# Optimization experiments

Hardware: AMD Instinct MI355X
Metric: run time of the kernel (lower is better)

Reference implementation:

```python
import jax, jax.numpy as jnp
import numpy as np
import math

D = 768
SCALE = math.sqrt(D)


def setup_inputs() -> dict:
    key = jax.random.key(0)
    k1, k2, k3, k4 = jax.random.split(key, 4)
    lhs = jax.random.normal(k1, (8, 1024, D), dtype=jnp.float32)
    rhs = jax.random.normal(k2, (8, 1024, D), dtype=jnp.float32)
    # xavier_normal_ std = sqrt(2/(fan_in+fan_out))
    std = math.sqrt(2.0 / (D + D))
    W_lhs = jax.random.normal(k3, (D, D), dtype=jnp.float32) * std
    W_rhs = jax.random.normal(k4, (D, D), dtype=jnp.float32) * std
    return {"lhs": lhs, "rhs": rhs, "W_lhs": W_lhs, "W_rhs": W_rhs}


def reference(lhs, rhs, W_lhs, W_rhs):
    # Linear (no bias): x @ W.T, then tanh
    l = jnp.tanh(jnp.einsum('nld,ed->nle', lhs, W_lhs))  # (N, L, D)
    r = jnp.tanh(jnp.einsum('nrd,ed->nre', rhs, W_rhs))  # (N, R, D)
    scores = jnp.einsum('nld,nrd->nlr', l, r)            # (N, L, R)
    attn_lhs = jax.nn.softmax(scores, axis=2)            # unscaled, row softmax
    attn_rhs = jax.nn.softmax(scores / SCALE, axis=1)    # scaled, column softmax
    out_lhs = jnp.einsum('nlr,nrd->nld', attn_lhs, rhs)
    out_rhs = jnp.einsum('nlr,nld->nrd', attn_rhs, lhs)
    return (jnp.concatenate([lhs, out_lhs], axis=2),
            jnp.concatenate([rhs, out_rhs], axis=2))
```

## Files before the change

kernel.cpp:

```cpp
#include <hip/hip_runtime.h>

typedef _Float16 f16_t;
typedef _Float16 f16x4 __attribute__((ext_vector_type(4)));
typedef _Float16 f16x8 __attribute__((ext_vector_type(8)));
typedef short s16x8 __attribute__((ext_vector_type(8)));
typedef unsigned short u16x4 __attribute__((ext_vector_type(4)));
typedef float floatx4 __attribute__((ext_vector_type(4)));

#define NB 8
#define SEQ 1024
#define DIM 768
#define INV_SCALE 0.03608439182435161f
#define ROW_SHIFT 40.0f

__device__ inline unsigned short f2bf(float f) {
  unsigned u = __builtin_bit_cast(unsigned, f);
  u += 0x7fffu + ((u >> 16) & 1u);
  return (unsigned short)(u >> 16);
}

__device__ inline void async_load16(const void* g, void* l) {
  __builtin_amdgcn_global_load_lds((__attribute__((address_space(1))) void*)g,
                                   (__attribute__((address_space(3))) void*)l,
                                   16, 0, 0);
}


__global__ __launch_bounds__(256, 3) void gemm_proj(
    const f16_t* __restrict__ A0, const f16_t* __restrict__ W0,
    const f16_t* __restrict__ A1, const f16_t* __restrict__ W1,
    f16_t* __restrict__ C0, f16_t* __restrict__ C1) {
  __shared__ __align__(16) f16_t sA[128 * 64];
  __shared__ __align__(16) f16_t sB[128 * 64];
  const int b = blockIdx.x;
  const int xcd = b & 7, slot = b >> 3;
  const int grp = slot / 6, j = slot - grp * 6;
  const int stripe = grp * 8 + xcd;
  const int z = stripe >> 6, my = stripe & 63;
  const f16_t* Ab = (z ? A1 : A0) + (size_t)my * 128 * DIM;
  const f16_t* Bb = (z ? W1 : W0) + (size_t)j * 128 * DIM;
  f16_t* C = z ? C1 : C0;
  const int tid = threadIdx.x;
  const int lane = tid & 63;
  const int wave = tid >> 6;
  const int wr = wave >> 1, wc = wave & 1;
  const int fr = lane & 15;
  const int fq = lane >> 4;
  const int swz = ((lane & 7) ^ (lane >> 3)) << 3;
  const int x7 = (fr & 7) << 3;

  floatx4 acc[4][4] = {};

  for (int kt = 0; kt < DIM; kt += 64) {
    #pragma unroll
    for (int i = 0; i < 4; ++i) {
      const int ch = i * 4 + wave;
      const int row = ch * 8 + (lane >> 3);
      const size_t g = (size_t)row * DIM + kt + swz;
      async_load16(Ab + g, (char*)sA + ch * 1024);
      async_load16(Bb + g, (char*)sB + ch * 1024);
    }
    __syncthreads();
    #pragma unroll
    for (int ks = 0; ks < 64; ks += 32) {
      f16x8 af[4], bf[4];
      #pragma unroll
      for (int t = 0; t < 4; ++t) {
        const int cs = (ks + fq * 8) ^ x7;
        af[t] = *(const f16x8*)&sA[(wr * 64 + t * 16 + fr) * 64 + cs];
        bf[t] = *(const f16x8*)&sB[(wc * 64 + t * 16 + fr) * 64 + cs];
      }
      #pragma unroll
      for (int ti = 0; ti < 4; ++ti)
        #pragma unroll
        for (int tj = 0; tj < 4; ++tj)
          acc[ti][tj] = __builtin_amdgcn_mfma_f32_16x16x32_f16(
              af[ti], bf[tj], acc[ti][tj], 0, 0, 0);
    }
    __syncthreads();
  }

  const size_t m0 = (size_t)my * 128, n0 = (size_t)j * 128;
  #pragma unroll
  for (int ti = 0; ti < 4; ++ti)
    #pragma unroll
    for (int tj = 0; tj < 4; ++tj) {
      const size_t gm = m0 + wr * 64 + ti * 16 + fq * 4;
      const size_t gn = n0 + wc * 64 + tj * 16 + fr;
      #pragma unroll
      for (int i = 0; i < 4; ++i)
        C[(gm + i) * DIM + gn] = (f16_t)tanhf(acc[ti][tj][i]);
    }
}

__global__ __launch_bounds__(256, 3) void gemm_scores(
    const f16_t* __restrict__ A, const f16_t* __restrict__ B,
    unsigned short* __restrict__ e_l, f16_t* __restrict__ e_rT,
    float* __restrict__ rowpart, float* __restrict__ colpart) {
  __shared__ __align__(16) f16_t sA[128 * 64];
  __shared__ __align__(16) f16_t sB[128 * 64];
  const int b = blockIdx.x;
  const int xcd = b & 7, slot = b >> 3;
  const int grp = slot >> 3, j = slot & 7;
  const int stripe = grp * 8 + xcd;
  const int z = stripe >> 3, my = stripe & 7;
  const f16_t* Ab = A + (size_t)z * SEQ * DIM + (size_t)my * 128 * DIM;
  const f16_t* Bb = B + (size_t)z * SEQ * DIM + (size_t)j * 128 * DIM;
  const int tid = threadIdx.x;
  const int lane = tid & 63;
  const int wave = tid >> 6;
  const int wr = wave >> 1, wc = wave & 1;
  const int fr = lane & 15;
  const int fq = lane >> 4;
  const int swz = ((lane & 7) ^ (lane >> 3)) << 3;
  const int x7 = (fr & 7) << 3;

  floatx4 acc[4][4] = {};

  for (int kt = 0; kt < DIM; kt += 64) {
    #pragma unroll
    for (int i = 0; i < 4; ++i) {
      const int ch = i * 4 + wave;
      const int row = ch * 8 + (lane >> 3);
      const size_t g = (size_t)row * DIM + kt + swz;
      async_load16(Ab + g, (char*)sA + ch * 1024);
      async_load16(Bb + g, (char*)sB + ch * 1024);
    }
    __syncthreads();
    #pragma unroll
    for (int ks = 0; ks < 64; ks += 32) {
      f16x8 af[4], bf[4];
      #pragma unroll
      for (int t = 0; t < 4; ++t) {
        const int cs = (ks + fq * 8) ^ x7;
        af[t] = *(const f16x8*)&sA[(wr * 64 + t * 16 + fr) * 64 + cs];
        bf[t] = *(const f16x8*)&sB[(wc * 64 + t * 16 + fr) * 64 + cs];
      }
      #pragma unroll
      for (int ti = 0; ti < 4; ++ti)
        #pragma unroll
        for (int tj = 0; tj < 4; ++tj)
          acc[ti][tj] = __builtin_amdgcn_mfma_f32_16x16x32_f16(
              af[ti], bf[tj], acc[ti][tj], 0, 0, 0);
    }
    __syncthreads();
  }

  const size_t m0 = (size_t)my * 128, n0 = (size_t)j * 128;
  unsigned short* eL = e_l + (size_t)z * SEQ * SEQ;
  f16_t* eT = e_rT + (size_t)z * SEQ * SEQ;
  float* srow = (float*)sA;
  float* scol = (float*)sB;

  #pragma unroll
  for (int ti = 0; ti < 4; ++ti) {
    #pragma unroll
    for (int i = 0; i < 4; ++i) {
      const size_t row = m0 + wr * 64 + ti * 16 + fq * 4 + i;
      float s = 0.f;
      #pragma unroll
      for (int tj = 0; tj < 4; ++tj) {
        const float e = __expf(acc[ti][tj][i] - ROW_SHIFT);
        s += e;
        eL[row * SEQ + n0 + wc * 64 + tj * 16 + fr] = f2bf(e);
      }
      s += __shfl_xor(s, 1, 64);
      s += __shfl_xor(s, 2, 64);
      s += __shfl_xor(s, 4, 64);
      s += __shfl_xor(s, 8, 64);
      if (fr == 0) srow[wc * 128 + wr * 64 + ti * 16 + fq * 4 + i] = s;
    }
  }
  #pragma unroll
  for (int tj = 0; tj < 4; ++tj) {
    const size_t coln = n0 + wc * 64 + tj * 16 + fr;
    float s = 0.f;
    #pragma unroll
    for (int ti = 0; ti < 4; ++ti) {
      f16x4 ev;
      #pragma unroll
      for (int i = 0; i < 4; ++i) {
        const float e = __expf(acc[ti][tj][i] * INV_SCALE);
        s += e;
        ev[i] = (f16_t)e;
      }
      *(f16x4*)&eT[coln * SEQ + m0 + wr * 64 + ti * 16 + fq * 4] = ev;
    }
    s += __shfl_xor(s, 16, 64);
    s += __shfl_xor(s, 32, 64);
    if (fq == 0) scol[wr * 128 + wc * 64 + tj * 16 + fr] = s;
  }
  __syncthreads();
  if (tid < 128)
    rowpart[((size_t)(z * 8 + j)) * SEQ + my * 128 + tid] =
        srow[tid] + srow[128 + tid];
  else
    colpart[((size_t)(z * 8 + my)) * SEQ + j * 128 + (tid - 128)] =
        scol[tid - 128] + scol[tid];
}

template <bool BF>
__device__ __forceinline__ void apply_body(
    const f16_t* __restrict__ Ab, const f16_t* __restrict__ Bb,
    float* __restrict__ C, const float* __restrict__ pp, f16_t* sA, f16_t* sB,
    float* sinv) {
  const int tid = threadIdx.x;
  const int lane = tid & 63;
  const int wave = tid >> 6;
  const int wr = wave >> 1, wc = wave & 1;
  const int fr = lane & 15;
  const int fq = lane >> 4;
  const int swz = ((lane & 7) ^ (lane >> 3)) << 3;
  const int x7 = (fr & 7) << 3;

  if (tid < 128) {
    float s = 0.f;
    #pragma unroll
    for (int k = 0; k < 8; ++k) s += pp[k * SEQ + tid];
    sinv[tid] = 1.f / s;
  }

  floatx4 acc[4][4] = {};

  for (int kt = 0; kt < SEQ; kt += 64) {
    #pragma unroll
    for (int i = 0; i < 4; ++i) {
      const int ch = i * 4 + wave;
      const int row = ch * 8 + (lane >> 3);
      const size_t g = (size_t)row * SEQ + kt + swz;
      async_load16(Ab + g, (char*)sA + ch * 1024);
      async_load16(Bb + g, (char*)sB + ch * 1024);
    }
    __syncthreads();
    #pragma unroll
    for (int ks = 0; ks < 64; ks += 32) {
      const int cs = (ks + fq * 8) ^ x7;
      #pragma unroll
      for (int ti = 0; ti < 4; ++ti) {
        const f16_t* pa = &sA[(wr * 64 + ti * 16 + fr) * 64 + cs];
        #pragma unroll
        for (int tj = 0; tj < 4; ++tj) {
          const f16_t* pb = &sB[(wc * 64 + tj * 16 + fr) * 64 + cs];
          if constexpr (BF)
            acc[ti][tj] = __builtin_amdgcn_mfma_f32_16x16x32_bf16(
                *(const s16x8*)pa, *(const s16x8*)pb, acc[ti][tj], 0, 0, 0);
          else
            acc[ti][tj] = __builtin_amdgcn_mfma_f32_16x16x32_f16(
                *(const f16x8*)pa, *(const f16x8*)pb, acc[ti][tj], 0, 0, 0);
        }
      }
    }
    __syncthreads();
  }

  #pragma unroll
  for (int ti = 0; ti < 4; ++ti) {
    const int gm = wr * 64 + ti * 16 + fq * 4;
    const floatx4 iv = *(const floatx4*)&sinv[gm];
    #pragma unroll
    for (int tj = 0; tj < 4; ++tj) {
      const int gn = wc * 64 + tj * 16 + fr;
      #pragma unroll
      for (int i = 0; i < 4; ++i)
        C[(size_t)(gm + i) * (2 * DIM) + gn] = acc[ti][tj][i] * iv[i];
    }
  }
}

__global__ __launch_bounds__(256, 3) void gemm_apply(
    const f16_t* __restrict__ e_l, const f16_t* __restrict__ e_rT,
    const f16_t* __restrict__ rhsT, const f16_t* __restrict__ lhsT,
    const float* __restrict__ rowpart, const float* __restrict__ colpart,
    float* __restrict__ out0, float* __restrict__ out1) {
  __shared__ __align__(16) f16_t sA[128 * 64];
  __shared__ __align__(16) f16_t sB[128 * 64];
  __shared__ __align__(16) float sinv[128];
  const int b = blockIdx.x;
  const int xcd = b & 7, slot = b >> 3;
  const int grp = slot / 6, j = slot - grp * 6;
  const int stripe = grp * 8 + xcd;
  const int z = stripe >> 3, my = stripe & 7;
  const int n = z & 7;
  const size_t m0 = (size_t)my * 128, n0 = (size_t)j * 128;
  if (z < 8) {
    apply_body<true>(e_l + (size_t)n * SEQ * SEQ + m0 * SEQ,
                     rhsT + (size_t)n * SEQ * DIM + n0 * SEQ,
                     out0 + (size_t)n * SEQ * 2 * DIM + DIM + m0 * 2 * DIM + n0,
                     rowpart + (size_t)n * 8 * SEQ + m0, sA, sB, sinv);
  } else {
    apply_body<false>(
        e_rT + (size_t)n * SEQ * SEQ + m0 * SEQ,
        lhsT + (size_t)n * SEQ * DIM + n0 * SEQ,
        out1 + (size_t)n * SEQ * 2 * DIM + DIM + m0 * 2 * DIM + n0,
        colpart + (size_t)n * 8 * SEQ + m0, sA, sB, sinv);
  }
}

__global__ __launch_bounds__(256) void prep(
    const float* __restrict__ lhs, const float* __restrict__ rhs,
    const float* __restrict__ Wl, const float* __restrict__ Wr,
    f16_t* __restrict__ lf, f16_t* __restrict__ rf, f16_t* __restrict__ lhsT,
    unsigned short* __restrict__ rhsT, f16_t* __restrict__ Wlh,
    f16_t* __restrict__ Wrh, float* __restrict__ o0, float* __restrict__ o1) {
  const int z = blockIdx.z;
  const int tid = threadIdx.x;
  const int x4 = (tid & 15) * 4, ty = tid >> 4;
  const int c0 = blockIdx.x * 64, r0 = blockIdx.y * 64;
  if (z >= 16) {
    if (blockIdx.y >= 12) return;
    const float* in = (z == 17 ? Wr : Wl);
    f16_t* out = (z == 17 ? Wrh : Wlh);
    #pragma unroll
    for (int it = 0; it < 4; ++it) {
      const int row = r0 + ty + it * 16;
      const float4 v = *(const float4*)&in[(size_t)row * DIM + c0 + x4];
      f16x4 h = {(f16_t)v.x, (f16_t)v.y, (f16_t)v.z, (f16_t)v.w};
      *(f16x4*)&out[(size_t)row * DIM + c0 + x4] = h;
    }
    return;
  }
  __shared__ float tile[64][65];
  const int n = z & 7;
  const float* in = (z < 8 ? lhs : rhs) + (size_t)n * SEQ * DIM;
  f16_t* fout = (z < 8 ? lf : rf) + (size_t)n * SEQ * DIM;
  float* oh = (z < 8 ? o0 : o1) + (size_t)n * SEQ * 2 * DIM;
  #pragma unroll
  for (int it = 0; it < 4; ++it) {
    const int row = ty + it * 16;
    const float4 v = *(const float4*)&in[(size_t)(r0 + row) * DIM + c0 + x4];
    f16x4 h = {(f16_t)v.x, (f16_t)v.y, (f16_t)v.z, (f16_t)v.w};
    *(f16x4*)&fout[(size_t)(r0 + row) * DIM + c0 + x4] = h;
    *(float4*)&oh[(size_t)(r0 + row) * 2 * DIM + c0 + x4] = v;
    tile[row][x4 + 0] = v.x;
    tile[row][x4 + 1] = v.y;
    tile[row][x4 + 2] = v.z;
    tile[row][x4 + 3] = v.w;
  }
  __syncthreads();
  if (z < 8) {
    f16_t* T = lhsT + (size_t)n * SEQ * DIM;
    #pragma unroll
    for (int it = 0; it < 4; ++it) {
      const int cr = ty + it * 16;
      f16x4 o = {(f16_t)tile[x4 + 0][cr], (f16_t)tile[x4 + 1][cr],
                 (f16_t)tile[x4 + 2][cr], (f16_t)tile[x4 + 3][cr]};
      *(f16x4*)&T[(size_t)(c0 + cr) * SEQ + r0 + x4] = o;
    }
  } else {
    unsigned short* T = rhsT + (size_t)n * SEQ * DIM;
    #pragma unroll
    for (int it = 0; it < 4; ++it) {
      const int cr = ty + it * 16;
      u16x4 o = {f2bf(tile[x4 + 0][cr]), f2bf(tile[x4 + 1][cr]),
                 f2bf(tile[x4 + 2][cr]), f2bf(tile[x4 + 3][cr])};
      *(u16x4*)&T[(size_t)(c0 + cr) * SEQ + r0 + x4] = o;
    }
  }
}

extern "C" void kernel_launch(void* const* d_in, const int* in_sizes, int n_in,
                              void* d_out, int out_size, void* d_ws,
                              size_t ws_size, hipStream_t stream) {
  const float* lhs = (const float*)d_in[0];
  const float* rhs = (const float*)d_in[1];
  const float* Wl = (const float*)d_in[2];
  const float* Wr = (const float*)d_in[3];
  float* out0 = (float*)d_out;
  float* out1 = out0 + (size_t)NB * SEQ * (2 * DIM);

  char* ws = (char*)d_ws;
  f16_t* lhsT = (f16_t*)(ws + 0);
  unsigned short* rhsT = (unsigned short*)(ws + 12582912);
  f16_t* l_f = (f16_t*)(ws + 25165824);
  f16_t* r_f = (f16_t*)(ws + 37748736);
  f16_t* lhs_f = (f16_t*)(ws + 50331648);
  f16_t* rhs_f = (f16_t*)(ws + 62914560);
  f16_t* Wl_h = (f16_t*)(ws + 75497472);
  f16_t* Wr_h = (f16_t*)(ws + 76677120);
  unsigned short* e_l = (unsigned short*)(ws + 50331648);
  f16_t* e_rT = (f16_t*)(ws + 67108864);
  float* rowpart = (float*)(ws + 83886080);
  float* colpart = (float*)(ws + 84148224);

  prep<<<dim3(12, 16, 18), 256, 0, stream>>>(lhs, rhs, Wl, Wr, lhs_f, rhs_f,
                                             lhsT, rhsT, Wl_h, Wr_h, out0,
                                             out1);
  gemm_proj<<<768, 256, 0, stream>>>(lhs_f, Wl_h, rhs_f, Wr_h, l_f, r_f);
  gemm_scores<<<512, 256, 0, stream>>>(l_f, r_f, e_l, e_rT, rowpart, colpart);
  gemm_apply<<<768, 256, 0, stream>>>((const f16_t*)e_l, e_rT,
                                      (const f16_t*)rhsT, lhsT, rowpart,
                                      colpart, out0, out1);
}
```

Before: 251.3 us.

## Move transposes into scores kernel, stage e_rT via LDS, simplify prep

Takes the lhs/rhs transposes out of the prep kernel and runs them as extra blocks inside the scores kernel, so that memory-bound work overlaps the compute-bound score GEMM. The e_rT transposed store now goes through a swizzled shared-memory tile, giving 16-byte coalesced writes. Row and column partial sums are written per wave-half (16 partials), which drops the shared-memory reduction. Block-to-XCD mapping is changed so that each batch sits on one XCD, and tanh is computed with exp plus rcp. The risks are uncoalesced scalar transpose stores in the new blocks and some precision loss from the approximate tanh.

```diff
diff --git a/kernel.cpp b/kernel.cpp
--- a/kernel.cpp
+++ b/kernel.cpp
@@ -4,7 +4,6 @@
 typedef _Float16 f16x4 __attribute__((ext_vector_type(4)));
 typedef _Float16 f16x8 __attribute__((ext_vector_type(8)));
 typedef short s16x8 __attribute__((ext_vector_type(8)));
-typedef unsigned short u16x4 __attribute__((ext_vector_type(4)));
 typedef float floatx4 __attribute__((ext_vector_type(4)));
 
 #define NB 8
@@ -33,13 +32,15 @@
   __shared__ __align__(16) f16_t sA[128 * 64];
   __shared__ __align__(16) f16_t sB[128 * 64];
   const int b = blockIdx.x;
-  const int xcd = b & 7, slot = b >> 3;
-  const int grp = slot / 6, j = slot - grp * 6;
-  const int stripe = grp * 8 + xcd;
-  const int z = stripe >> 6, my = stripe & 63;
-  const f16_t* Ab = (z ? A1 : A0) + (size_t)my * 128 * DIM;
-  const f16_t* Bb = (z ? W1 : W0) + (size_t)j * 128 * DIM;
-  f16_t* C = z ? C1 : C0;
+  const int n = b & 7;
+  const int s = b >> 3;
+  const int side = s / 48;
+  const int t = s - side * 48;
+  const int myb = t / 6, j = t - myb * 6;
+  const int my = n * 8 + myb;
+  const f16_t* Ab = (side ? A1 : A0) + (size_t)my * 128 * DIM;
+  const f16_t* Bb = (side ? W1 : W0) + (size_t)j * 128 * DIM;
+  f16_t* C = side ? C1 : C0;
   const int tid = threadIdx.x;
   const int lane = tid & 63;
   const int wave = tid >> 6;
@@ -65,10 +66,10 @@
     for (int ks = 0; ks < 64; ks += 32) {
       f16x8 af[4], bf[4];
       #pragma unroll
-      for (int t = 0; t < 4; ++t) {
+      for (int t2 = 0; t2 < 4; ++t2) {
         const int cs = (ks + fq * 8) ^ x7;
-        af[t] = *(const f16x8*)&sA[(wr * 64 + t * 16 + fr) * 64 + cs];
-        bf[t] = *(const f16x8*)&sB[(wc * 64 + t * 16 + fr) * 64 + cs];
+        af[t2] = *(const f16x8*)&sA[(wr * 64 + t2 * 16 + fr) * 64 + cs];
+        bf[t2] = *(const f16x8*)&sB[(wc * 64 + t2 * 16 + fr) * 64 + cs];
       }
       #pragma unroll
       for (int ti = 0; ti < 4; ++ti)
@@ -88,25 +89,59 @@
       const size_t gm = m0 + wr * 64 + ti * 16 + fq * 4;
       const size_t gn = n0 + wc * 64 + tj * 16 + fr;
       #pragma unroll
-      for (int i = 0; i < 4; ++i)
-        C[(gm + i) * DIM + gn] = (f16_t)tanhf(acc[ti][tj][i]);
-    }
-}
-
-__global__ __launch_bounds__(256, 3) void gemm_scores(
+      for (int i = 0; i < 4; ++i) {
+        const float e = __expf(2.f * acc[ti][tj][i]);
+        C[(gm + i) * DIM + gn] =
+            (f16_t)(1.f - 2.f * __builtin_amdgcn_rcpf(e + 1.f));
+      }
+    }
+}
+
+__global__ __launch_bounds__(256, 3) void scores_mix(
     const f16_t* __restrict__ A, const f16_t* __restrict__ B,
+    const float* __restrict__ lhs32, const float* __restrict__ rhs32,
     unsigned short* __restrict__ e_l, f16_t* __restrict__ e_rT,
+    f16_t* __restrict__ lhsT, unsigned short* __restrict__ rhsT,
     float* __restrict__ rowpart, float* __restrict__ colpart) {
-  __shared__ __align__(16) f16_t sA[128 * 64];
-  __shared__ __align__(16) f16_t sB[128 * 64];
+  __shared__ __align__(16) char smem[32768];
   const int b = blockIdx.x;
-  const int xcd = b & 7, slot = b >> 3;
-  const int grp = slot >> 3, j = slot & 7;
-  const int stripe = grp * 8 + xcd;
-  const int z = stripe >> 3, my = stripe & 7;
+  const int tid = threadIdx.x;
+
+  if (b >= 512) {
+    float(*tile)[65] = (float(*)[65])smem;
+    const int t = b - 512;
+    const int side = t >> 7;
+    const int n = (t >> 4) & 7, r0 = (t & 15) * 64;
+    const float* in = (side ? rhs32 : lhs32) + (size_t)n * SEQ * DIM;
+    const int x = tid & 63, y = tid >> 6;
+    for (int d0 = 0; d0 < DIM; d0 += 64) {
+      #pragma unroll
+      for (int yy = y; yy < 64; yy += 4)
+        tile[yy][x] = in[(size_t)(r0 + yy) * DIM + d0 + x];
+      __syncthreads();
+      if (side == 0) {
+        f16_t* out = lhsT + (size_t)n * SEQ * DIM;
+        #pragma unroll
+        for (int yy = y; yy < 64; yy += 4)
+          out[(size_t)(d0 + yy) * SEQ + r0 + x] = (f16_t)tile[x][yy];
+      } else {
+        unsigned short* out = rhsT + (size_t)n * SEQ * DIM;
+        #pragma unroll
+        for (int yy = y; yy < 64; yy += 4)
+          out[(size_t)(d0 + yy) * SEQ + r0 + x] = f2bf(tile[x][yy]);
+      }
+      __syncthreads();
+    }
+    return;
+  }
+
+  f16_t* sA = (f16_t*)smem;
+  f16_t* sB = sA + 8192;
+  const int z = b & 7;
+  const int s = b >> 3;
+  const int my = s >> 3, j = s & 7;
   const f16_t* Ab = A + (size_t)z * SEQ * DIM + (size_t)my * 128 * DIM;
   const f16_t* Bb = B + (size_t)z * SEQ * DIM + (size_t)j * 128 * DIM;
-  const int tid = threadIdx.x;
   const int lane = tid & 63;
   const int wave = tid >> 6;
   const int wr = wave >> 1, wc = wave & 1;
@@ -131,10 +166,10 @@
     for (int ks = 0; ks < 64; ks += 32) {
       f16x8 af[4], bf[4];
       #pragma unroll
-      for (int t = 0; t < 4; ++t) {
+      for (int t2 = 0; t2 < 4; ++t2) {
         const int cs = (ks + fq * 8) ^ x7;
-        af[t] = *(const f16x8*)&sA[(wr * 64 + t * 16 + fr) * 64 + cs];
-        bf[t] = *(const f16x8*)&sB[(wc * 64 + t * 16 + fr) * 64 + cs];
+        af[t2] = *(const f16x8*)&sA[(wr * 64 + t2 * 16 + fr) * 64 + cs];
+        bf[t2] = *(const f16x8*)&sB[(wc * 64 + t2 * 16 + fr) * 64 + cs];
       }
       #pragma unroll
       for (int ti = 0; ti < 4; ++ti)
@@ -149,54 +184,54 @@
   const size_t m0 = (size_t)my * 128, n0 = (size_t)j * 128;
   unsigned short* eL = e_l + (size_t)z * SEQ * SEQ;
   f16_t* eT = e_rT + (size_t)z * SEQ * SEQ;
-  float* srow = (float*)sA;
-  float* scol = (float*)sB;
 
   #pragma unroll
   for (int ti = 0; ti < 4; ++ti) {
     #pragma unroll
     for (int i = 0; i < 4; ++i) {
-      const size_t row = m0 + wr * 64 + ti * 16 + fq * 4 + i;
-      float s = 0.f;
+      const int rloc = wr * 64 + ti * 16 + fq * 4 + i;
+      float sum = 0.f;
       #pragma unroll
       for (int tj = 0; tj < 4; ++tj) {
         const float e = __expf(acc[ti][tj][i] - ROW_SHIFT);
-        s += e;
-        eL[row * SEQ + n0 + wc * 64 + tj * 16 + fr] = f2bf(e);
-      }
-      s += __shfl_xor(s, 1, 64);
-      s += __shfl_xor(s, 2, 64);
-      s += __shfl_xor(s, 4, 64);
-      s += __shfl_xor(s, 8, 64);
-      if (fr == 0) srow[wc * 128 + wr * 64 + ti * 16 + fq * 4 + i] = s;
+        sum += e;
+        eL[(m0 + rloc) * SEQ + n0 + wc * 64 + tj * 16 + fr] = f2bf(e);
+      }
+      sum += __shfl_xor(sum, 1, 64);
+      sum += __shfl_xor(sum, 2, 64);
+      sum += __shfl_xor(sum, 4, 64);
+      sum += __shfl_xor(sum, 8, 64);
+      if (fr == 0)
+        rowpart[((size_t)(z * 16 + j * 2 + wc)) * SEQ + m0 + rloc] = sum;
     }
   }
   #pragma unroll
   for (int tj = 0; tj < 4; ++tj) {
-    const size_t coln = n0 + wc * 64 + tj * 16 + fr;
-    float s = 0.f;
+    const int rp = wc * 64 + tj * 16 + fr;
+    float sum = 0.f;
     #pragma unroll
     for (int ti = 0; ti < 4; ++ti) {
-      f16x4 ev;
       #pragma unroll
       for (int i = 0; i < 4; ++i) {
         const float e = __expf(acc[ti][tj][i] * INV_SCALE);
-        s += e;
-        ev[i] = (f16_t)e;
-      }
-      *(f16x4*)&eT[coln * SEQ + m0 + wr * 64 + ti * 16 + fq * 4] = ev;
-    }
-    s += __shfl_xor(s, 16, 64);
-    s += __shfl_xor(s, 32, 64);
-    if (fq == 0) scol[wr * 128 + wc * 64 + tj * 16 + fr] = s;
+        sum += e;
+        const int cp = wr * 64 + ti * 16 + fq * 4 + i;
+        *(f16_t*)(smem + rp * 256 + ((cp * 2) ^ ((rp & 7) << 4))) = (f16_t)e;
+      }
+    }
+    sum += __shfl_xor(sum, 16, 64);
+    sum += __shfl_xor(sum, 32, 64);
+    if (fq == 0)
+      colpart[((size_t)(z * 16 + my * 2 + wr)) * SEQ + n0 + rp] = sum;
   }
   __syncthreads();
-  if (tid < 128)
-    rowpart[((size_t)(z * 8 + j)) * SEQ + my * 128 + tid] =
-        srow[tid] + srow[128 + tid];
-  else
-    colpart[((size_t)(z * 8 + my)) * SEQ + j * 128 + (tid - 128)] =
-        scol[tid - 128] + scol[tid];
+  #pragma unroll
+  for (int it = 0; it < 8; ++it) {
+    const int r = it * 16 + (tid >> 4), chunk = tid & 15;
+    const f16x8 v =
+        *(const f16x8*)(smem + r * 256 + ((chunk * 16) ^ ((r & 7) << 4)));
+    *(f16x8*)&eT[(n0 + r) * SEQ + m0 + chunk * 8] = v;
+  }
 }
 
 template <bool BF>
@@ -216,7 +251,7 @@
   if (tid < 128) {
     float s = 0.f;
     #pragma unroll
-    for (int k = 0; k < 8; ++k) s += pp[k * SEQ + tid];
+    for (int k = 0; k < 16; ++k) s += pp[k * SEQ + tid];
     sinv[tid] = 1.f / s;
   }
 
@@ -276,86 +311,52 @@
   __shared__ __align__(16) f16_t sB[128 * 64];
   __shared__ __align__(16) float sinv[128];
   const int b = blockIdx.x;
-  const int xcd = b & 7, slot = b >> 3;
-  const int grp = slot / 6, j = slot - grp * 6;
-  const int stripe = grp * 8 + xcd;
-  const int z = stripe >> 3, my = stripe & 7;
-  const int n = z & 7;
+  const int n = b & 7;
+  const int s = b >> 3;
+  const int side = s / 48;
+  const int t = s - side * 48;
+  const int my = t / 6, j = t - my * 6;
   const size_t m0 = (size_t)my * 128, n0 = (size_t)j * 128;
-  if (z < 8) {
+  if (side == 0) {
     apply_body<true>(e_l + (size_t)n * SEQ * SEQ + m0 * SEQ,
                      rhsT + (size_t)n * SEQ * DIM + n0 * SEQ,
                      out0 + (size_t)n * SEQ * 2 * DIM + DIM + m0 * 2 * DIM + n0,
-                     rowpart + (size_t)n * 8 * SEQ + m0, sA, sB, sinv);
+                     rowpart + (size_t)n * 16 * SEQ + m0, sA, sB, sinv);
   } else {
     apply_body<false>(
         e_rT + (size_t)n * SEQ * SEQ + m0 * SEQ,
         lhsT + (size_t)n * SEQ * DIM + n0 * SEQ,
         out1 + (size_t)n * SEQ * 2 * DIM + DIM + m0 * 2 * DIM + n0,
-        colpart + (size_t)n * 8 * SEQ + m0, sA, sB, sinv);
+        colpart + (size_t)n * 16 * SEQ + m0, sA, sB, sinv);
   }
 }
 
 __global__ __launch_bounds__(256) void prep(
     const float* __restrict__ lhs, const float* __restrict__ rhs,
     const float* __restrict__ Wl, const float* __restrict__ Wr,
-    f16_t* __restrict__ lf, f16_t* __restrict__ rf, f16_t* __restrict__ lhsT,
-    unsigned short* __restrict__ rhsT, f16_t* __restrict__ Wlh,
+    f16_t* __restrict__ lf, f16_t* __restrict__ rf, f16_t* __restrict__ Wlh,
     f16_t* __restrict__ Wrh, float* __restrict__ o0, float* __restrict__ o1) {
-  const int z = blockIdx.z;
-  const int tid = threadIdx.x;
-  const int x4 = (tid & 15) * 4, ty = tid >> 4;
-  const int c0 = blockIdx.x * 64, r0 = blockIdx.y * 64;
-  if (z >= 16) {
-    if (blockIdx.y >= 12) return;
-    const float* in = (z == 17 ? Wr : Wl);
-    f16_t* out = (z == 17 ? Wrh : Wlh);
-    #pragma unroll
-    for (int it = 0; it < 4; ++it) {
-      const int row = r0 + ty + it * 16;
-      const float4 v = *(const float4*)&in[(size_t)row * DIM + c0 + x4];
-      f16x4 h = {(f16_t)v.x, (f16_t)v.y, (f16_t)v.z, (f16_t)v.w};
-      *(f16x4*)&out[(size_t)row * DIM + c0 + x4] = h;
-    }
+  const int which = blockIdx.y;
+  const int bx = blockIdx.x;
+  if (bx >= 6144) {
+    const float4* in = (const float4*)(which ? Wr : Wl);
+    f16_t* out = which ? Wrh : Wlh;
+    const int idx = (bx - 6144) * 256 + threadIdx.x;
+    const float4 v = in[idx];
+    f16x4 h = {(f16_t)v.x, (f16_t)v.y, (f16_t)v.z, (f16_t)v.w};
+    *(f16x4*)(out + idx * 4) = h;
     return;
   }
-  __shared__ float tile[64][65];
-  const int n = z & 7;
-  const float* in = (z < 8 ? lhs : rhs) + (size_t)n * SEQ * DIM;
-  f16_t* fout = (z < 8 ? lf : rf) + (size_t)n * SEQ * DIM;
-  float* oh = (z < 8 ? o0 : o1) + (size_t)n * SEQ * 2 * DIM;
-  #pragma unroll
-  for (int it = 0; it < 4; ++it) {
-    const int row = ty + it * 16;
-    const float4 v = *(const float4*)&in[(size_t)(r0 + row) * DIM + c0 + x4];
-    f16x4 h = {(f16_t)v.x, (f16_t)v.y, (f16_t)v.z, (f16_t)v.w};
-    *(f16x4*)&fout[(size_t)(r0 + row) * DIM + c0 + x4] = h;
-    *(float4*)&oh[(size_t)(r0 + row) * 2 * DIM + c0 + x4] = v;
-    tile[row][x4 + 0] = v.x;
-    tile[row][x4 + 1] = v.y;
-    tile[row][x4 + 2] = v.z;
-    tile[row][x4 + 3] = v.w;
-  }
-  __syncthreads();
-  if (z < 8) {
-    f16_t* T = lhsT + (size_t)n * SEQ * DIM;
-    #pragma unroll
-    for (int it = 0; it < 4; ++it) {
-      const int cr = ty + it * 16;
-      f16x4 o = {(f16_t)tile[x4 + 0][cr], (f16_t)tile[x4 + 1][cr],
-                 (f16_t)tile[x4 + 2][cr], (f16_t)tile[x4 + 3][cr]};
-      *(f16x4*)&T[(size_t)(c0 + cr) * SEQ + r0 + x4] = o;
-    }
-  } else {
-    unsigned short* T = rhsT + (size_t)n * SEQ * DIM;
-    #pragma unroll
-    for (int it = 0; it < 4; ++it) {
-      const int cr = ty + it * 16;
-      u16x4 o = {f2bf(tile[x4 + 0][cr]), f2bf(tile[x4 + 1][cr]),
-                 f2bf(tile[x4 + 2][cr]), f2bf(tile[x4 + 3][cr])};
-      *(u16x4*)&T[(size_t)(c0 + cr) * SEQ + r0 + x4] = o;
-    }
-  }
+  const float4* in = (const float4*)(which ? rhs : lhs);
+  f16_t* out = which ? rf : lf;
+  float* outh = which ? o1 : o0;
+  const int idx = bx * 256 + threadIdx.x;
+  const float4 v = in[idx];
+  const int i4 = idx * 4;
+  f16x4 h = {(f16_t)v.x, (f16_t)v.y, (f16_t)v.z, (f16_t)v.w};
+  *(f16x4*)(out + i4) = h;
+  const int row = i4 / DIM, col = i4 % DIM;
+  *(float4*)&outh[(size_t)row * (2 * DIM) + col] = v;
 }
 
 extern "C" void kernel_launch(void* const* d_in, const int* in_sizes, int n_in,
@@ -380,13 +381,13 @@
   unsigned short* e_l = (unsigned short*)(ws + 50331648);
   f16_t* e_rT = (f16_t*)(ws + 67108864);
   float* rowpart = (float*)(ws + 83886080);
-  float* colpart = (float*)(ws + 84148224);
-
-  prep<<<dim3(12, 16, 18), 256, 0, stream>>>(lhs, rhs, Wl, Wr, lhs_f, rhs_f,
-                                             lhsT, rhsT, Wl_h, Wr_h, out0,
-                                             out1);
+  float* colpart = (float*)(ws + 84410368);
+
+  prep<<<dim3(6720, 2), 256, 0, stream>>>(lhs, rhs, Wl, Wr, lhs_f, rhs_f,
+                                          Wl_h, Wr_h, out0, out1);
   gemm_proj<<<768, 256, 0, stream>>>(lhs_f, Wl_h, rhs_f, Wr_h, l_f, r_f);
-  gemm_scores<<<512, 256, 0, stream>>>(l_f, r_f, e_l, e_rT, rowpart, colpart);
+  scores_mix<<<768, 256, 0, stream>>>(l_f, r_f, lhs, rhs, e_l, e_rT, lhsT,
+                                      rhsT, rowpart, colpart);
   gemm_apply<<<768, 256, 0, stream>>>((const f16_t*)e_l, e_rT,
                                       (const f16_t*)rhsT, lhsT, rowpart,
                                       colpart, out0, out1);
```

New measurement: 242.8 us. -3.4%, faster.
